# Kernel tuning notes

Measured on AMD Instinct MI355X. Metric: run time of the kernel, lower is better.

The kernel has to match this reference:

```python
import jax, jax.numpy as jnp
import numpy as np

H = W = 32          # gussin() is hard-coded to width=32 in BASE
C = 512             # BASE inner_nc; down conv is 1024->512
V = 1.5             # gaussian sigma


def _gaussian_weights():
    # Vectorized equivalent of gussin(1.5): g[p, x, y] for p = i*W + k,
    # g = exp(-((x-i)^2+(y-k)^2)/(2 v^2)) / (2 pi v^2), normalized per p.
    idx = np.arange(H, dtype=np.float64)
    d1 = (idx[:, None] - idx[None, :]) ** 2            # (i, x)
    d2 = d1[:, None, :, None] + d1[None, :, None, :]    # (i, k, x, y)
    g = np.exp(-d2 / (2.0 * V * V)) / (2.0 * np.pi * V * V)
    g = g.reshape(H * W, H, W)
    g = g / g.sum(axis=(1, 2), keepdims=True)
    return jnp.asarray(g, dtype=jnp.float32)


def _instance_norm(x, eps=1e-5):
    # InstanceNorm2d(affine=False): per-(b,c) mean/biased-var over (h,w)
    mu = x.mean(axis=(2, 3), keepdims=True)
    var = jnp.mean((x - mu) ** 2, axis=(2, 3), keepdims=True)
    return (x - mu) / jnp.sqrt(var + eps)


def _patches3(fm):
    # fm: (C, H+2, W+2) zero-padded map -> 3x3 patches: (H*W, C, 3, 3)
    p = jnp.stack([fm[:, di:di + H, dj:dj + W]
                   for di in range(3) for dj in range(3)], axis=-1)  # (C,H,W,9)
    return p.transpose(1, 2, 0, 3).reshape(H * W, C, 3, 3)


def setup_inputs() -> dict:
    key = jax.random.key(0)
    ks = jax.random.split(key, 4)
    x = jax.random.normal(ks[0], (1, C, H, W), jnp.float32)
    w_se1 = jax.random.normal(ks[1], (C // 16, C), jnp.float32) * 0.05   # SE squeeze fc
    w_se2 = jax.random.normal(ks[2], (C, C // 16), jnp.float32) * 0.05   # SE excite fc
    w_down = jax.random.normal(ks[3], (C, 2 * C, 1, 1), jnp.float32) * 0.05  # 1x1 conv 1024->512
    return {"x": x, "w_se1": w_se1, "w_se2": w_se2, "w_down": w_down}


def reference(x, w_se1, w_se2, w_down):
    gus = _gaussian_weights()                                # (HW, H, W), constant
    # --- SELayer(512, 16) ---
    s = x.mean(axis=(2, 3))                                  # (1, C) global avg pool
    s = jax.nn.relu(s @ w_se1.T)                             # (1, C/16)
    s = jax.nn.sigmoid(s @ w_se2.T)                          # (1, C)
    out32 = x * s[:, :, None, None]                          # (1, C, H, W)
    # --- gaussian-weighted pooling (einsum instead of (HW,C,H,W) broadcast) ---
    gus_out = jnp.einsum('pxy,cxy->pc', gus, out32[0])       # (HW, C)
    gus_out = gus_out.reshape(1, C, H, W)                    # raw reshape, as in torch .view
    # --- patch-based contextual self-attention (CSA) ---
    sig = jax.nn.sigmoid(out32)                              # (1, C, H, W)
    sig_pad = jnp.pad(sig[0], ((0, 0), (1, 1), (1, 1)))
    raw_pad = jnp.pad(out32[0], ((0, 0), (1, 1), (1, 1)))
    p_sig = _patches3(sig_pad)                               # (HW, C, 3, 3)
    p_raw = _patches3(raw_pad)                               # (HW, C, 3, 3)
    center = sig[0].transpose(1, 2, 0).reshape(H * W, C, 1, 1)  # center sigmoid vec per loc
    score = jnp.mean(center * p_sig, axis=1)                 # (HW, 3, 3)
    attn = jax.nn.softmax(score.reshape(H * W, 9), axis=1).reshape(H * W, 1, 3, 3)
    out_csa = jnp.sum(attn * p_raw, axis=(2, 3))             # (HW, C)
    out_csa = out_csa.reshape(1, C, H, W)                    # raw reshape, as in torch .view
    # --- concat + 1x1 conv down + InstanceNorm + LeakyReLU(0.2) ---
    cat = jnp.concatenate([gus_out, out_csa], axis=1)        # (1, 2C, H, W)
    y = jnp.einsum('bihw,oi->bohw', cat, w_down[:, :, 0, 0])
    y = _instance_norm(y)
    return jnp.where(y >= 0, y, 0.2 * y)
```

## Files before the change

kernel.cpp:

```cpp
#include <hip/hip_runtime.h>


typedef short short8 __attribute__((ext_vector_type(8)));
typedef short short4v __attribute__((ext_vector_type(4)));
typedef float floatx4 __attribute__((ext_vector_type(4)));
typedef float floatx16 __attribute__((ext_vector_type(16)));

__device__ __forceinline__ unsigned short f2bf(float x) {
  union { float f; unsigned u; } v; v.f = x;
  unsigned u = v.u;
  u = (u + 0x7fffu + ((u >> 16) & 1u)) >> 16;
  return (unsigned short)u;
}

__device__ __forceinline__ float dot4(float4 a, float4 b) {
  return a.x * b.x + a.y * b.y + a.z * b.z + a.w * b.w;
}

__device__ __forceinline__ float block_reduce_256(float v, float* sm4) {
  #pragma unroll
  for (int off = 32; off >= 1; off >>= 1) v += __shfl_down(v, off);
  __syncthreads();
  if ((threadIdx.x & 63) == 0) sm4[threadIdx.x >> 6] = v;
  __syncthreads();
  return sm4[0] + sm4[1] + sm4[2] + sm4[3];
}

__device__ __forceinline__ void gauss_lds(float* g, int tid) {
  int ga = tid >> 3, gb0 = (tid & 7) * 4;
  float e[4]; float gs = 0.0f;
  #pragma unroll
  for (int q = 0; q < 4; q++) {
    float d = (float)(ga - (gb0 + q));
    e[q] = __expf(d * d * (-1.0f / 4.5f));
    gs += e[q];
  }
  gs += __shfl_xor(gs, 1, 8);
  gs += __shfl_xor(gs, 2, 8);
  gs += __shfl_xor(gs, 4, 8);
  float ginv = 1.0f / gs;
  #pragma unroll
  for (int q = 0; q < 4; q++) g[ga * 32 + gb0 + q] = e[q] * ginv;
}

__global__ void k_mean_cvt(const float* __restrict__ x, float* __restrict__ smean,
                           const float* __restrict__ wdn, unsigned short* __restrict__ Abf) {
  if (blockIdx.x >= 512) {
    int base = (blockIdx.x - 512) * 2048 + threadIdx.x * 8;
    float4 a = *(const float4*)&wdn[base];
    float4 b = *(const float4*)&wdn[base + 4];
    short8 s;
    s[0] = (short)f2bf(a.x); s[1] = (short)f2bf(a.y); s[2] = (short)f2bf(a.z); s[3] = (short)f2bf(a.w);
    s[4] = (short)f2bf(b.x); s[5] = (short)f2bf(b.y); s[6] = (short)f2bf(b.z); s[7] = (short)f2bf(b.w);
    *(short8*)&Abf[base] = s;
    return;
  }
  __shared__ float sm4[4];
  int c = blockIdx.x;
  const float4* row = (const float4*)(x + c * 1024);
  float4 v = row[threadIdx.x];
  float s = v.x + v.y + v.z + v.w;
  float t = block_reduce_256(s, sm4);
  if (threadIdx.x == 0) smean[c] = t * (1.0f / 1024.0f);
}

__global__ void k_apply(const float* __restrict__ x, const float* __restrict__ smean,
                        const float* __restrict__ w1, const float* __restrict__ w2,
                        float* __restrict__ out32, float* __restrict__ out32T,
                        float* __restrict__ sigT) {
  __shared__ float sm[512];
  __shared__ float s1[32];
  __shared__ float sc[32];
  __shared__ float tile[32][33];
  int tid = threadIdx.x;
  for (int i = tid; i < 512; i += 256) sm[i] = smean[i];
  __syncthreads();
  int j = tid >> 3, l8 = tid & 7;
  float a = 0.0f;
  for (int cc = l8; cc < 512; cc += 8) a += sm[cc] * w1[j * 512 + cc];
  a += __shfl_down(a, 4, 8);
  a += __shfl_down(a, 2, 8);
  a += __shfl_down(a, 1, 8);
  if (l8 == 0) s1[j] = fmaxf(a, 0.0f);
  __syncthreads();
  int c0 = blockIdx.y * 32, hw0 = blockIdx.x * 32;
  if (tid < 32) {
    float bb = 0.0f;
    #pragma unroll
    for (int jj = 0; jj < 32; jj++) bb += s1[jj] * w2[(c0 + tid) * 32 + jj];
    sc[tid] = 1.0f / (1.0f + __expf(-bb));
  }
  __syncthreads();
  int tx = tid & 31, ty = tid >> 5;
  #pragma unroll
  for (int r = 0; r < 4; r++) {
    int c = ty + 8 * r;
    float v = x[(c0 + c) * 1024 + hw0 + tx] * sc[c];
    out32[(c0 + c) * 1024 + hw0 + tx] = v;
    tile[c][tx] = v;
  }
  __syncthreads();
  #pragma unroll
  for (int r = 0; r < 4; r++) {
    int hw = hw0 + ty + 8 * r;
    float v = tile[tx][ty + 8 * r];
    out32T[hw * 512 + c0 + tx] = v;
    sigT[hw * 512 + c0 + tx] = 1.0f / (1.0f + __expf(-v));
  }
}

__global__ void k_gausscsa(const float* __restrict__ out32, const float* __restrict__ sigT,
                           const float* __restrict__ out32T, unsigned short* __restrict__ catT) {
  if (blockIdx.x < 512) {
    __shared__ float g[1024];
    __shared__ float row[32 * 36];
    __shared__ float T[32 * 36];
    int c = blockIdx.x;
    int tid = threadIdx.x;
    gauss_lds(g, tid);
    {
      int xx = tid >> 3, y4 = tid & 7;
      float4 v = *(const float4*)&out32[c * 1024 + xx * 32 + y4 * 4];
      *(float4*)&row[xx * 36 + y4 * 4] = v;
    }
    __syncthreads();
    {
      int xx = tid & 31, kg = tid >> 5;
      int k0 = kg * 4;
      const float4* rw4 = (const float4*)(row + xx * 36);
      float s0 = 0, s1 = 0, s2 = 0, s3 = 0;
      #pragma unroll
      for (int y4 = 0; y4 < 8; y4++) {
        float4 rv = rw4[y4];
        s0 += dot4(*(const float4*)&g[(k0 + 0) * 32 + y4 * 4], rv);
        s1 += dot4(*(const float4*)&g[(k0 + 1) * 32 + y4 * 4], rv);
        s2 += dot4(*(const float4*)&g[(k0 + 2) * 32 + y4 * 4], rv);
        s3 += dot4(*(const float4*)&g[(k0 + 3) * 32 + y4 * 4], rv);
      }
      T[(k0 + 0) * 36 + xx] = s0;
      T[(k0 + 1) * 36 + xx] = s1;
      T[(k0 + 2) * 36 + xx] = s2;
      T[(k0 + 3) * 36 + xx] = s3;
    }
    __syncthreads();
    {
      int i = tid >> 3;
      int sub = tid & 7;
      int par = sub & 1, kq = sub >> 1;
      int kb = kq * 8 + par;
      float s0 = 0, s1 = 0, s2 = 0, s3 = 0;
      #pragma unroll
      for (int x4 = 0; x4 < 8; x4++) {
        float4 gv = *(const float4*)&g[i * 32 + x4 * 4];
        s0 += dot4(gv, *(const float4*)&T[(kb + 0) * 36 + x4 * 4]);
        s1 += dot4(gv, *(const float4*)&T[(kb + 2) * 36 + x4 * 4]);
        s2 += dot4(gv, *(const float4*)&T[(kb + 4) * 36 + x4 * 4]);
        s3 += dot4(gv, *(const float4*)&T[(kb + 6) * 36 + x4 * 4]);
      }
      short4v o;
      o[0] = (short)f2bf(s0); o[1] = (short)f2bf(s1);
      o[2] = (short)f2bf(s2); o[3] = (short)f2bf(s3);
      *(short4v*)&catT[(par * 512 + c) * 1024 + i * 16 + kq * 4] = o;
    }
  } else {
    int wv = threadIdx.x >> 6;
    int lane = threadIdx.x & 63;
    int p = (blockIdx.x - 512) * 4 + wv;
    int h = p >> 5, w = p & 31;
    int c0 = lane * 8;
    float4 ce0 = *(const float4*)&sigT[p * 512 + c0];
    float4 ce1 = *(const float4*)&sigT[p * 512 + c0 + 4];
    int qoff[9];
    float s[9];
    #pragma unroll
    for (int dd = 0; dd < 9; dd++) {
      int hh = h + dd / 3 - 1, ww = w + (dd % 3) - 1;
      bool v = (hh >= 0) && (hh < 32) && (ww >= 0) && (ww < 32);
      qoff[dd] = v ? (hh * 32 + ww) * 512 : -1;
      float a = 0.0f;
      if (v) {
        float4 n0 = *(const float4*)&sigT[qoff[dd] + c0];
        float4 n1 = *(const float4*)&sigT[qoff[dd] + c0 + 4];
        a = dot4(ce0, n0) + dot4(ce1, n1);
      }
      #pragma unroll
      for (int off = 32; off >= 1; off >>= 1) a += __shfl_xor(a, off);
      s[dd] = a;
    }
    float mx = -1e30f;
    #pragma unroll
    for (int dd = 0; dd < 9; dd++) { s[dd] *= (1.0f / 512.0f); mx = fmaxf(mx, s[dd]); }
    float tot = 0.0f;
    #pragma unroll
    for (int dd = 0; dd < 9; dd++) { s[dd] = __expf(s[dd] - mx); tot += s[dd]; }
    float inv = 1.0f / tot;
    float o[8] = {0, 0, 0, 0, 0, 0, 0, 0};
    #pragma unroll
    for (int dd = 0; dd < 9; dd++) {
      if (qoff[dd] >= 0) {
        float att = s[dd] * inv;
        float4 r0 = *(const float4*)&out32T[qoff[dd] + c0];
        float4 r1 = *(const float4*)&out32T[qoff[dd] + c0 + 4];
        o[0] += att * r0.x; o[1] += att * r0.y; o[2] += att * r0.z; o[3] += att * r0.w;
        o[4] += att * r1.x; o[5] += att * r1.y; o[6] += att * r1.z; o[7] += att * r1.w;
      }
    }
    int kcol = 512 + (p >> 1);
    int nbase = (p & 1) * 512 + c0;
    #pragma unroll
    for (int q = 0; q < 8; q++) catT[(nbase + q) * 1024 + kcol] = f2bf(o[q]);
  }
}

__global__ void k_gemm(const unsigned short* __restrict__ Abf,
                       const unsigned short* __restrict__ Bbf,
                       float* __restrict__ y) {
  __shared__ float red[3][1024];
  int tid = threadIdx.x;
  int wv = tid >> 6, lane = tid & 63;
  int bm = (blockIdx.x >> 5) * 32;
  int nn = (blockIdx.x & 31) * 32;
  int l32 = lane & 31, half = lane >> 5;
  const short8* ap = (const short8*)(Abf + (bm + l32) * 1024 + wv * 256 + half * 8);
  const short8* bp = (const short8*)(Bbf + (nn + l32) * 1024 + wv * 256 + half * 8);
  floatx16 acc = {};
  #pragma unroll
  for (int ks = 0; ks < 16; ks++) {
    short8 a = ap[ks * 2];
    short8 b = bp[ks * 2];
    acc = __builtin_amdgcn_mfma_f32_32x32x16_bf16(a, b, acc, 0, 0, 0);
  }
  if (wv != 0) {
    #pragma unroll
    for (int r4 = 0; r4 < 4; r4++) {
      float4 v = make_float4(acc[r4 * 4], acc[r4 * 4 + 1], acc[r4 * 4 + 2], acc[r4 * 4 + 3]);
      *(float4*)&red[wv - 1][lane * 16 + r4 * 4] = v;
    }
  }
  __syncthreads();
  if (wv == 0) {
    #pragma unroll
    for (int r = 0; r < 16; r++) {
      float v = acc[r] + red[0][lane * 16 + r] + red[1][lane * 16 + r] + red[2][lane * 16 + r];
      int rowm = (r & 3) + 8 * (r >> 2) + 4 * half;
      y[(bm + rowm) * 1024 + nn + l32] = v;
    }
  }
}

__global__ void k_inorm(const float* __restrict__ y, float* __restrict__ out) {
  __shared__ float sm4[4];
  __shared__ float vrow[1024];
  int o = blockIdx.x;
  int tid = threadIdx.x;
  float4 v4 = *(const float4*)&y[o * 1024 + tid * 4];
  *(float4*)&vrow[tid * 4] = v4;
  float s = v4.x + v4.y + v4.z + v4.w;
  float q = v4.x * v4.x + v4.y * v4.y + v4.z * v4.z + v4.w * v4.w;
  float ts = block_reduce_256(s, sm4);
  float tq = block_reduce_256(q, sm4);
  float mean = ts * (1.0f / 1024.0f);
  float var = tq * (1.0f / 1024.0f) - mean * mean;
  float inv = rsqrtf(var + 1e-5f);
  float4 w4 = *(const float4*)&vrow[tid * 4];
  float4 r4;
  float a0 = (w4.x - mean) * inv; r4.x = a0 >= 0.0f ? a0 : 0.2f * a0;
  float a1 = (w4.y - mean) * inv; r4.y = a1 >= 0.0f ? a1 : 0.2f * a1;
  float a2 = (w4.z - mean) * inv; r4.z = a2 >= 0.0f ? a2 : 0.2f * a2;
  float a3 = (w4.w - mean) * inv; r4.w = a3 >= 0.0f ? a3 : 0.2f * a3;
  *(float4*)&out[o * 1024 + tid * 4] = r4;
}

extern "C" void kernel_launch(void* const* d_in, const int* in_sizes, int n_in,
                              void* d_out, int out_size, void* d_ws, size_t ws_size,
                              hipStream_t stream) {
  const float* x      = (const float*)d_in[0];
  const float* w_se1  = (const float*)d_in[1];
  const float* w_se2  = (const float*)d_in[2];
  const float* w_down = (const float*)d_in[3];
  float* out = (float*)d_out;

  float* ws = (float*)d_ws;
  float* smean  = ws;
  float* out32  = ws + 1024;
  float* out32T = ws + 525312;
  float* sigT   = ws + 1049600;
  unsigned short* catT = (unsigned short*)(ws + 1573888);
  unsigned short* Abf  = (unsigned short*)(ws + 2098176);
  float* ybuf   = ws + 2360320;

  k_mean_cvt<<<768, 256, 0, stream>>>(x, smean, w_down, Abf);
  k_apply<<<dim3(32, 16), 256, 0, stream>>>(x, smean, w_se1, w_se2, out32, out32T, sigT);
  k_gausscsa<<<768, 256, 0, stream>>>(out32, sigT, out32T, catT);
  k_gemm<<<512, 256, 0, stream>>>(Abf, catT, ybuf);
  k_inorm<<<512, 256, 0, stream>>>(ybuf, out);
}
```

Before: 100.3 us.

## Drop sigT buffer, recompute sigmoid in CSA, move weight cast into apply kernel

```diff
diff --git a/kernel.cpp b/kernel.cpp
--- a/kernel.cpp
+++ b/kernel.cpp
@@ -3,7 +3,6 @@
 
 typedef short short8 __attribute__((ext_vector_type(8)));
 typedef short short4v __attribute__((ext_vector_type(4)));
-typedef float floatx4 __attribute__((ext_vector_type(4)));
 typedef float floatx16 __attribute__((ext_vector_type(16)));
 
 __device__ __forceinline__ unsigned short f2bf(float x) {
@@ -17,6 +16,10 @@
   return a.x * b.x + a.y * b.y + a.z * b.z + a.w * b.w;
 }
 
+__device__ __forceinline__ float sigm(float x) {
+  return 1.0f / (1.0f + __expf(-x));
+}
+
 __device__ __forceinline__ float block_reduce_256(float v, float* sm4) {
   #pragma unroll
   for (int off = 32; off >= 1; off >>= 1) v += __shfl_down(v, off);
@@ -43,10 +46,23 @@
   for (int q = 0; q < 4; q++) g[ga * 32 + gb0 + q] = e[q] * ginv;
 }
 
-__global__ void k_mean_cvt(const float* __restrict__ x, float* __restrict__ smean,
-                           const float* __restrict__ wdn, unsigned short* __restrict__ Abf) {
+__global__ void k_mean(const float* __restrict__ x, float* __restrict__ smean) {
+  __shared__ float sm4[4];
+  int c = blockIdx.x;
+  const float4* row = (const float4*)(x + c * 1024);
+  float4 v = row[threadIdx.x];
+  float s = v.x + v.y + v.z + v.w;
+  float t = block_reduce_256(s, sm4);
+  if (threadIdx.x == 0) smean[c] = t * (1.0f / 1024.0f);
+}
+
+__global__ void k_apply(const float* __restrict__ x, const float* __restrict__ smean,
+                        const float* __restrict__ w1, const float* __restrict__ w2,
+                        const float* __restrict__ wdn, unsigned short* __restrict__ Abf,
+                        float* __restrict__ out32, float* __restrict__ out32T) {
+  int tid = threadIdx.x;
   if (blockIdx.x >= 512) {
-    int base = (blockIdx.x - 512) * 2048 + threadIdx.x * 8;
+    int base = (blockIdx.x - 512) * 2048 + tid * 8;
     float4 a = *(const float4*)&wdn[base];
     float4 b = *(const float4*)&wdn[base + 4];
     short8 s;
@@ -55,24 +71,10 @@
     *(short8*)&Abf[base] = s;
     return;
   }
-  __shared__ float sm4[4];
-  int c = blockIdx.x;
-  const float4* row = (const float4*)(x + c * 1024);
-  float4 v = row[threadIdx.x];
-  float s = v.x + v.y + v.z + v.w;
-  float t = block_reduce_256(s, sm4);
-  if (threadIdx.x == 0) smean[c] = t * (1.0f / 1024.0f);
-}
-
-__global__ void k_apply(const float* __restrict__ x, const float* __restrict__ smean,
-                        const float* __restrict__ w1, const float* __restrict__ w2,
-                        float* __restrict__ out32, float* __restrict__ out32T,
-                        float* __restrict__ sigT) {
   __shared__ float sm[512];
   __shared__ float s1[32];
   __shared__ float sc[32];
   __shared__ float tile[32][33];
-  int tid = threadIdx.x;
   for (int i = tid; i < 512; i += 256) sm[i] = smean[i];
   __syncthreads();
   int j = tid >> 3, l8 = tid & 7;
@@ -83,12 +85,12 @@
   a += __shfl_down(a, 1, 8);
   if (l8 == 0) s1[j] = fmaxf(a, 0.0f);
   __syncthreads();
-  int c0 = blockIdx.y * 32, hw0 = blockIdx.x * 32;
+  int c0 = (blockIdx.x & 15) * 32, hw0 = (blockIdx.x >> 4) * 32;
   if (tid < 32) {
     float bb = 0.0f;
     #pragma unroll
     for (int jj = 0; jj < 32; jj++) bb += s1[jj] * w2[(c0 + tid) * 32 + jj];
-    sc[tid] = 1.0f / (1.0f + __expf(-bb));
+    sc[tid] = sigm(bb);
   }
   __syncthreads();
   int tx = tid & 31, ty = tid >> 5;
@@ -103,14 +105,12 @@
   #pragma unroll
   for (int r = 0; r < 4; r++) {
     int hw = hw0 + ty + 8 * r;
-    float v = tile[tx][ty + 8 * r];
-    out32T[hw * 512 + c0 + tx] = v;
-    sigT[hw * 512 + c0 + tx] = 1.0f / (1.0f + __expf(-v));
-  }
-}
-
-__global__ void k_gausscsa(const float* __restrict__ out32, const float* __restrict__ sigT,
-                           const float* __restrict__ out32T, unsigned short* __restrict__ catT) {
+    out32T[hw * 512 + c0 + tx] = tile[tx][ty + 8 * r];
+  }
+}
+
+__global__ void k_gausscsa(const float* __restrict__ out32, const float* __restrict__ out32T,
+                           unsigned short* __restrict__ catT) {
   if (blockIdx.x < 512) {
     __shared__ float g[1024];
     __shared__ float row[32 * 36];
@@ -168,8 +168,10 @@
     int p = (blockIdx.x - 512) * 4 + wv;
     int h = p >> 5, w = p & 31;
     int c0 = lane * 8;
-    float4 ce0 = *(const float4*)&sigT[p * 512 + c0];
-    float4 ce1 = *(const float4*)&sigT[p * 512 + c0 + 4];
+    float4 cr0 = *(const float4*)&out32T[p * 512 + c0];
+    float4 cr1 = *(const float4*)&out32T[p * 512 + c0 + 4];
+    float4 ce0 = make_float4(sigm(cr0.x), sigm(cr0.y), sigm(cr0.z), sigm(cr0.w));
+    float4 ce1 = make_float4(sigm(cr1.x), sigm(cr1.y), sigm(cr1.z), sigm(cr1.w));
     int qoff[9];
     float s[9];
     #pragma unroll
@@ -179,9 +181,11 @@
       qoff[dd] = v ? (hh * 32 + ww) * 512 : -1;
       float a = 0.0f;
       if (v) {
-        float4 n0 = *(const float4*)&sigT[qoff[dd] + c0];
-        float4 n1 = *(const float4*)&sigT[qoff[dd] + c0 + 4];
-        a = dot4(ce0, n0) + dot4(ce1, n1);
+        float4 n0 = *(const float4*)&out32T[qoff[dd] + c0];
+        float4 n1 = *(const float4*)&out32T[qoff[dd] + c0 + 4];
+        float4 sg0 = make_float4(sigm(n0.x), sigm(n0.y), sigm(n0.z), sigm(n0.w));
+        float4 sg1 = make_float4(sigm(n1.x), sigm(n1.y), sigm(n1.z), sigm(n1.w));
+        a = dot4(ce0, sg0) + dot4(ce1, sg1);
       }
       #pragma unroll
       for (int off = 32; off >= 1; off >>= 1) a += __shfl_xor(a, off);
@@ -284,14 +288,13 @@
   float* smean  = ws;
   float* out32  = ws + 1024;
   float* out32T = ws + 525312;
-  float* sigT   = ws + 1049600;
-  unsigned short* catT = (unsigned short*)(ws + 1573888);
-  unsigned short* Abf  = (unsigned short*)(ws + 2098176);
-  float* ybuf   = ws + 2360320;
-
-  k_mean_cvt<<<768, 256, 0, stream>>>(x, smean, w_down, Abf);
-  k_apply<<<dim3(32, 16), 256, 0, stream>>>(x, smean, w_se1, w_se2, out32, out32T, sigT);
-  k_gausscsa<<<768, 256, 0, stream>>>(out32, sigT, out32T, catT);
+  unsigned short* catT = (unsigned short*)(ws + 1049600);
+  unsigned short* Abf  = (unsigned short*)(ws + 1573888);
+  float* ybuf   = ws + 1836032;
+
+  k_mean<<<512, 256, 0, stream>>>(x, smean);
+  k_apply<<<768, 256, 0, stream>>>(x, smean, w_se1, w_se2, w_down, Abf, out32, out32T);
+  k_gausscsa<<<768, 256, 0, stream>>>(out32, out32T, catT);
   k_gemm<<<512, 256, 0, stream>>>(Abf, catT, ybuf);
   k_inorm<<<512, 256, 0, stream>>>(ybuf, out);
 }
```

After: 101.2 us. About the same (+0.9%).
